# Kernel tuning notes

Hardware: AMD Instinct MI355X
Metric: run time of the kernel (lower is better)

Reference implementation:

```python
import jax, jax.numpy as jnp
import numpy as np

HID = 4

def setup_inputs() -> dict:
    key = jax.random.key(0)
    ks = jax.random.split(key, 8)
    B, T, F = 4096, 512, 16
    x = jax.random.normal(ks[0], (B, T, F), dtype=jnp.float32)
    # Keras LSTMCell params: kernel [F,4H], recurrent_kernel [H,4H], bias [4H] (gate order i,f,c,o)
    Wk = jax.random.normal(ks[1], (F, 4 * HID), dtype=jnp.float32) * 0.1
    Wr = jax.random.normal(ks[2], (HID, 4 * HID), dtype=jnp.float32) * 0.1
    b = jnp.zeros((4 * HID,), dtype=jnp.float32)
    W1 = jax.random.normal(ks[3], (HID, 64), dtype=jnp.float32) * 0.1
    b1 = jnp.zeros((64,), dtype=jnp.float32)
    W2 = jax.random.normal(ks[4], (64, 5), dtype=jnp.float32) * 0.1
    b2 = jnp.zeros((5,), dtype=jnp.float32)
    return {"x": x, "Wk": Wk, "Wr": Wr, "b": b, "W1": W1, "b1": b1, "W2": W2, "b2": b2}

def _lstm_last_h(x, Wk, Wr, b):
    B = x.shape[0]
    # precompute input projections for all timesteps: [T, B, 4H]
    xg = jnp.einsum('btf,fg->tbg', x, Wk) + b

    def step(carry, xg_t):
        h, c = carry
        gates = xg_t + h @ Wr  # [B, 4H]
        i, f, g, o = jnp.split(gates, 4, axis=-1)
        i = jax.nn.sigmoid(i)
        f = jax.nn.sigmoid(f)
        o = jax.nn.sigmoid(o)
        c = f * c + i * jnp.tanh(g)
        h = o * jnp.tanh(c)
        return (h, c), None

    h0 = jnp.zeros((B, HID), dtype=x.dtype)
    c0 = jnp.zeros((B, HID), dtype=x.dtype)
    (h, _), _ = jax.lax.scan(step, (h0, c0), xg)
    return h  # [B, H] -- RNN returns last output only (return_sequences=False)

def reference(x, Wk, Wr, b, W1, b1, W2, b2):
    h = _lstm_last_h(x, Wk, Wr, b)
    h = jax.nn.relu(h @ W1 + b1)
    return jax.nn.softmax(h @ W2 + b2, axis=-1)  # [B, 5]
```

## Files before the change

### kernel.cpp

```cpp
#include <hip/hip_runtime.h>

#define TLEN 512
#define LOG2E 1.44269504088896340736f

#if __has_builtin(__builtin_amdgcn_exp2f)
#define EXP2F(x) __builtin_amdgcn_exp2f(x)
#else
#define EXP2F(x) __exp2f(x)
#endif
#if __has_builtin(__builtin_amdgcn_rcpf)
#define RCPF(x) __builtin_amdgcn_rcpf(x)
#else
#define RCPF(x) (1.0f / (x))
#endif

#define SWZ(v, xm) __int_as_float(__builtin_amdgcn_ds_swizzle(__float_as_int(v), (((xm) << 10) | 0x1F)))
#define DPPF(v, ctrl) __int_as_float(__builtin_amdgcn_update_dpp(__float_as_int(v), __float_as_int(v), (ctrl), 0xF, 0xF, false))
#define QB(v, k) DPPF(v, 0x55 * (k))
#define XOR3(v)  DPPF(v, 0x1B)
#define XOR7(v)  DPPF(v, 0x141)
#define XOR8(v)  DPPF(v, 0x128)

struct X4 { float4 a, b, c, d; };

__global__ __launch_bounds__(256, 1) void lstm_mlp_kernel(
    const float* __restrict__ x,
    const float* __restrict__ Wk,
    const float* __restrict__ Wr,
    const float* __restrict__ bg,
    const float* __restrict__ W1,
    const float* __restrict__ b1,
    const float* __restrict__ W2,
    const float* __restrict__ b2,
    float* __restrict__ out,
    int B)
{
    const int tid = blockIdx.x * 256 + threadIdx.x;
    const int seq = tid >> 4;
    if (seq >= B) return;
    const int i16 = tid & 15;
    const int j   = i16 >> 2;
    const int q   = i16 & 3;
    const int gate = q * 4 + j;

    const bool is_g = (q == 2);
    const float k1 = is_g ? (-2.0f * LOG2E) : (-LOG2E);
    const float m1c = is_g ? (-4.0f * LOG2E) : 1.0f;
    const float m0c = is_g ? (2.0f * LOG2E) : 0.0f;

    float wk[16];
#pragma unroll
    for (int f = 0; f < 16; ++f) wk[f] = k1 * Wk[f * 16 + gate];
    const float wr0 = k1 * Wr[(j ^ 0) * 16 + gate];
    const float wr1 = k1 * Wr[(j ^ 1) * 16 + gate];
    const float wr2 = k1 * Wr[(j ^ 2) * 16 + gate];
    const float wr3 = k1 * Wr[(j ^ 3) * 16 + gate];
    const float biasS = k1 * bg[gate];

    const X4* xt = reinterpret_cast<const X4*>(x) + (size_t)seq * TLEN;

    float cs = 0.0f, h = 0.0f;

#define DOT4S(v, w0_, w1_, w2_, w3_, seed) \
    fmaf((v).x, (w0_), fmaf((v).y, (w1_), fmaf((v).z, (w2_), fmaf((v).w, (w3_), (seed)))))
#define DOTB(Bk) \
    ((DOT4S((Bk).a, wk[0], wk[1], wk[2], wk[3], biasS) + \
      DOT4S((Bk).b, wk[4], wk[5], wk[6], wk[7], 0.0f)) + \
     (DOT4S((Bk).c, wk[8], wk[9], wk[10], wk[11], 0.0f) + \
      DOT4S((Bk).d, wk[12], wk[13], wk[14], wk[15], 0.0f)))

#define STEP(XD) { \
    float h1_ = XOR7(XOR3(h));    \
    float h2_ = XOR8(h);          \
    float h3_ = XOR8(h1_);        \
    float pre = fmaf(h, wr0, (XD)); \
    pre = fmaf(h2_, wr2, pre); \
    pre = fmaf(h1_, wr1, pre); \
    pre = fmaf(h3_, wr3, pre); \
    float r_ = RCPF(1.0f + EXP2F(pre)); \
    float av = fmaf(m1c, r_, m0c); \
    float iv = QB(av, 0); \
    float fv = QB(av, 1); \
    float gv = QB(av, 2); \
    float ov = QB(av, 3); \
    cs = fmaf(fv, cs, iv * gv); \
    float th_ = fmaf(2.0f, RCPF(1.0f + EXP2F(cs)), -1.0f); \
    h = ov * th_; }

    X4 B0 = xt[0], B1 = xt[1], B2 = xt[2], B3 = xt[3];
    X4 B4 = xt[4], B5 = xt[5], B6 = xt[6], B7 = xt[7];

    for (int t = 0; t < TLEN - 8; t += 8) {
        { float xd = DOTB(B0); B0 = xt[t +  8]; STEP(xd); }
        { float xd = DOTB(B1); B1 = xt[t +  9]; STEP(xd); }
        { float xd = DOTB(B2); B2 = xt[t + 10]; STEP(xd); }
        { float xd = DOTB(B3); B3 = xt[t + 11]; STEP(xd); }
        { float xd = DOTB(B4); B4 = xt[t + 12]; STEP(xd); }
        { float xd = DOTB(B5); B5 = xt[t + 13]; STEP(xd); }
        { float xd = DOTB(B6); B6 = xt[t + 14]; STEP(xd); }
        { float xd = DOTB(B7); B7 = xt[t + 15]; STEP(xd); }
    }
    { float xd = DOTB(B0); STEP(xd); }
    { float xd = DOTB(B1); STEP(xd); }
    { float xd = DOTB(B2); STEP(xd); }
    { float xd = DOTB(B3); STEP(xd); }
    { float xd = DOTB(B4); STEP(xd); }
    { float xd = DOTB(B5); STEP(xd); }
    { float xd = DOTB(B6); STEP(xd); }
    { float xd = DOTB(B7); STEP(xd); }

    float hA = h;
    float hB = SWZ(h, 4), hC = SWZ(h, 8), hD = SWZ(h, 12);

    float p0 = 0.f, p1 = 0.f, p2 = 0.f, p3 = 0.f, p4 = 0.f;
#pragma unroll
    for (int r = 0; r < 4; ++r) {
        const int u = i16 * 4 + r;
        float acc = b1[u];
        acc = fmaf(hA, W1[(j ^ 0) * 64 + u], acc);
        acc = fmaf(hB, W1[(j ^ 1) * 64 + u], acc);
        acc = fmaf(hC, W1[(j ^ 2) * 64 + u], acc);
        acc = fmaf(hD, W1[(j ^ 3) * 64 + u], acc);
        acc = fmaxf(acc, 0.0f);
        p0 = fmaf(acc, W2[u * 5 + 0], p0);
        p1 = fmaf(acc, W2[u * 5 + 1], p1);
        p2 = fmaf(acc, W2[u * 5 + 2], p2);
        p3 = fmaf(acc, W2[u * 5 + 3], p3);
        p4 = fmaf(acc, W2[u * 5 + 4], p4);
    }
    p0 += SWZ(p0, 1); p1 += SWZ(p1, 1); p2 += SWZ(p2, 1); p3 += SWZ(p3, 1); p4 += SWZ(p4, 1);
    p0 += SWZ(p0, 2); p1 += SWZ(p1, 2); p2 += SWZ(p2, 2); p3 += SWZ(p3, 2); p4 += SWZ(p4, 2);
    p0 += SWZ(p0, 4); p1 += SWZ(p1, 4); p2 += SWZ(p2, 4); p3 += SWZ(p3, 4); p4 += SWZ(p4, 4);
    p0 += SWZ(p0, 8); p1 += SWZ(p1, 8); p2 += SWZ(p2, 8); p3 += SWZ(p3, 8); p4 += SWZ(p4, 8);

    p0 += b2[0]; p1 += b2[1]; p2 += b2[2]; p3 += b2[3]; p4 += b2[4];

    float mx = fmaxf(fmaxf(fmaxf(p0, p1), fmaxf(p2, p3)), p4);
    float e0 = EXP2F((p0 - mx) * LOG2E);
    float e1 = EXP2F((p1 - mx) * LOG2E);
    float e2 = EXP2F((p2 - mx) * LOG2E);
    float e3 = EXP2F((p3 - mx) * LOG2E);
    float e4 = EXP2F((p4 - mx) * LOG2E);
    float s = ((e0 + e1) + (e2 + e3)) + e4;
    float rs = RCPF(s);

    if (i16 == 0) {
        float* op = out + (size_t)seq * 5;
        op[0] = e0 * rs; op[1] = e1 * rs; op[2] = e2 * rs;
        op[3] = e3 * rs; op[4] = e4 * rs;
    }
}

extern "C" void kernel_launch(void* const* d_in, const int* in_sizes, int n_in,
                              void* d_out, int out_size, void* d_ws, size_t ws_size,
                              hipStream_t stream) {
    const float* x  = (const float*)d_in[0];
    const float* Wk = (const float*)d_in[1];
    const float* Wr = (const float*)d_in[2];
    const float* bg = (const float*)d_in[3];
    const float* W1 = (const float*)d_in[4];
    const float* b1 = (const float*)d_in[5];
    const float* W2 = (const float*)d_in[6];
    const float* b2 = (const float*)d_in[7];
    float* out = (float*)d_out;

    const int B = in_sizes[0] / (TLEN * 16);
    const int threads = B * 16;
    dim3 block(256);
    dim3 grid((threads + 255) / 256);
    lstm_mlp_kernel<<<grid, block, 0, stream>>>(x, Wk, Wr, bg, W1, b1, W2, b2, out, B);
}
```

Before: 73.54 us.

## Stream LSTM inputs via async global_load_lds into a 4-slot LDS ring

Replaces the per-thread register prefetch of 8 timesteps (each thread loading the full 64-byte row of x) with direct global-to-LDS loads. Each wave cooperatively fetches 4 timesteps for its 4 sequences into a rotating 4-slot LDS buffer, and readiness is tracked with manual s_waitcnt vmcnt. The aim is to cut redundant global loads and register pressure, since the 16 lanes of a sequence previously each fetched the same x row. In exchange it relies on hand-placed waitcnt correctness with no LDS barrier, drops the bounds check on seq, and assumes B is divisible by 16.

```diff
diff --git a/kernel.cpp b/kernel.cpp
--- a/kernel.cpp
+++ b/kernel.cpp
@@ -21,7 +21,10 @@
 #define XOR7(v)  DPPF(v, 0x141)
 #define XOR8(v)  DPPF(v, 0x128)
 
-struct X4 { float4 a, b, c, d; };
+#define WAITVM(N) asm volatile("s_waitcnt vmcnt(" #N ")" ::: "memory")
+
+typedef const __attribute__((address_space(1))) unsigned int gu32;
+typedef __attribute__((address_space(3))) unsigned int lu32;
 
 __global__ __launch_bounds__(256, 1) void lstm_mlp_kernel(
     const float* __restrict__ x,
@@ -35,10 +38,13 @@
     float* __restrict__ out,
     int B)
 {
-    const int tid = blockIdx.x * 256 + threadIdx.x;
-    const int seq = tid >> 4;
-    if (seq >= B) return;
-    const int i16 = tid & 15;
+    __shared__ float4 lds[4][4][64];
+
+    const int tidx = threadIdx.x;
+    const int w   = tidx >> 6;
+    const int L   = tidx & 63;
+    const int sl  = (tidx >> 4) & 3;
+    const int i16 = tidx & 15;
     const int j   = i16 >> 2;
     const int q   = i16 & 3;
     const int gate = q * 4 + j;
@@ -57,17 +63,31 @@
     const float wr3 = k1 * Wr[(j ^ 3) * 16 + gate];
     const float biasS = k1 * bg[gate];
 
-    const X4* xt = reinterpret_cast<const X4*>(x) + (size_t)seq * TLEN;
+    const int dseq = L & 3;
+    const int dtl  = L >> 4;
+    const int chnk = (L >> 2) & 3;
+    const float* xb = x + ((size_t)(blockIdx.x * 16 + w * 4 + dseq) * TLEN + dtl) * 16 + chnk * 4;
+
+#define DMA(SLOT, T0) \
+    __builtin_amdgcn_global_load_lds((gu32*)(const void*)(xb + (size_t)(T0) * 16), \
+                                     (lu32*)(void*)(&lds[w][SLOT][0]), 16, 0, 0)
+
+    const float4* __restrict__ lw = &lds[w][0][0];
 
     float cs = 0.0f, h = 0.0f;
 
 #define DOT4S(v, w0_, w1_, w2_, w3_, seed) \
     fmaf((v).x, (w0_), fmaf((v).y, (w1_), fmaf((v).z, (w2_), fmaf((v).w, (w3_), (seed)))))
-#define DOTB(Bk) \
-    ((DOT4S((Bk).a, wk[0], wk[1], wk[2], wk[3], biasS) + \
-      DOT4S((Bk).b, wk[4], wk[5], wk[6], wk[7], 0.0f)) + \
-     (DOT4S((Bk).c, wk[8], wk[9], wk[10], wk[11], 0.0f) + \
-      DOT4S((Bk).d, wk[12], wk[13], wk[14], wk[15], 0.0f)))
+
+#define RD_DOT(BASE, OFF, DST) { \
+    float4 ra_ = (BASE)[(OFF) + sl]; \
+    float4 rb_ = (BASE)[(OFF) + sl + 4]; \
+    float4 rc_ = (BASE)[(OFF) + sl + 8]; \
+    float4 rd_ = (BASE)[(OFF) + sl + 12]; \
+    DST = (DOT4S(ra_, wk[0], wk[1], wk[2], wk[3], biasS) + \
+           DOT4S(rb_, wk[4], wk[5], wk[6], wk[7], 0.0f)) + \
+          (DOT4S(rc_, wk[8], wk[9], wk[10], wk[11], 0.0f) + \
+           DOT4S(rd_, wk[12], wk[13], wk[14], wk[15], 0.0f)); }
 
 #define STEP(XD) { \
     float h1_ = XOR7(XOR3(h));    \
@@ -87,27 +107,30 @@
     float th_ = fmaf(2.0f, RCPF(1.0f + EXP2F(cs)), -1.0f); \
     h = ov * th_; }
 
-    X4 B0 = xt[0], B1 = xt[1], B2 = xt[2], B3 = xt[3];
-    X4 B4 = xt[4], B5 = xt[5], B6 = xt[6], B7 = xt[7];
+    WAITVM(0);
+    DMA(0, 0);
+    DMA(1, 4);
+    DMA(2, 8);
+    DMA(3, 12);
+    WAITVM(3);
+    float xd;
+    RD_DOT(lw, 0, xd);
 
-    for (int t = 0; t < TLEN - 8; t += 8) {
-        { float xd = DOTB(B0); B0 = xt[t +  8]; STEP(xd); }
-        { float xd = DOTB(B1); B1 = xt[t +  9]; STEP(xd); }
-        { float xd = DOTB(B2); B2 = xt[t + 10]; STEP(xd); }
-        { float xd = DOTB(B3); B3 = xt[t + 11]; STEP(xd); }
-        { float xd = DOTB(B4); B4 = xt[t + 12]; STEP(xd); }
-        { float xd = DOTB(B5); B5 = xt[t + 13]; STEP(xd); }
-        { float xd = DOTB(B6); B6 = xt[t + 14]; STEP(xd); }
-        { float xd = DOTB(B7); B7 = xt[t + 15]; STEP(xd); }
+#pragma clang loop unroll(disable)
+    for (int g = 0; g < 128; ++g) {
+        WAITVM(2);
+        const float4* lg  = lw + ((g & 3) << 6);
+        const float4* lg1 = lw + (((g + 1) & 3) << 6);
+        float xdn;
+        RD_DOT(lg, 16, xdn); STEP(xd); xd = xdn;
+        RD_DOT(lg, 32, xdn); STEP(xd); xd = xdn;
+        RD_DOT(lg, 48, xdn); STEP(xd); xd = xdn;
+        RD_DOT(lg1, 0, xdn); STEP(xd); xd = xdn;
+        int t0 = (g + 4) << 2;
+        t0 = t0 > (TLEN - 4) ? (TLEN - 4) : t0;
+        DMA(g & 3, t0);
     }
-    { float xd = DOTB(B0); STEP(xd); }
-    { float xd = DOTB(B1); STEP(xd); }
-    { float xd = DOTB(B2); STEP(xd); }
-    { float xd = DOTB(B3); STEP(xd); }
-    { float xd = DOTB(B4); STEP(xd); }
-    { float xd = DOTB(B5); STEP(xd); }
-    { float xd = DOTB(B6); STEP(xd); }
-    { float xd = DOTB(B7); STEP(xd); }
+    WAITVM(0);
 
     float hA = h;
     float hB = SWZ(h, 4), hC = SWZ(h, 8), hD = SWZ(h, 12);
@@ -145,6 +168,7 @@
     float rs = RCPF(s);
 
     if (i16 == 0) {
+        const int seq = blockIdx.x * 16 + (tidx >> 4);
         float* op = out + (size_t)seq * 5;
         op[0] = e0 * rs; op[1] = e1 * rs; op[2] = e2 * rs;
         op[3] = e3 * rs; op[4] = e4 * rs;
@@ -165,8 +189,7 @@
     float* out = (float*)d_out;
 
     const int B = in_sizes[0] / (TLEN * 16);
-    const int threads = B * 16;
     dim3 block(256);
-    dim3 grid((threads + 255) / 256);
+    dim3 grid(B / 16);
     lstm_mlp_kernel<<<grid, block, 0, stream>>>(x, Wk, Wr, bg, W1, b1, W2, b2, out, B);
 }
```

Measured after the change: 110.1 us. 1.5x slower.
